# Performance work log

Hardware: AMD Instinct MI355X
Metric: run time of the kernel (lower is better)

Reference implementation:

```python
import jax, jax.numpy as jnp
import numpy as np

IN_DIM, EDGE_DIM, HID = 128, 64, 128
N_A, N_B, E_AB, E_AA = 50000, 50000, 320000, 320000


def setup_inputs() -> dict:
    key = jax.random.key(0)
    ks = jax.random.split(key, 13)
    inv = lambda n: 1.0 / np.sqrt(n)
    return {
        "x_a": jax.random.normal(ks[0], (N_A, IN_DIM), jnp.float32),
        "x_b": jax.random.normal(ks[1], (N_B, IN_DIM), jnp.float32),
        "ei_ab": jax.random.randint(ks[2], (2, E_AB), 0, N_A),
        "ea_ab": jax.random.normal(ks[3], (E_AB, EDGE_DIM), jnp.float32),
        "ei_aa": jax.random.randint(ks[4], (2, E_AA), 0, N_A),
        "ea_aa": jax.random.normal(ks[5], (E_AA, EDGE_DIM), jnp.float32),
        "Wh_w": jax.random.normal(ks[6], (EDGE_DIM, HID), jnp.float32) * inv(EDGE_DIM),
        "Wh_b": jnp.zeros((HID,), jnp.float32),
        "Wn_w": jax.random.normal(ks[7], (2 * IN_DIM, HID), jnp.float32) * inv(2 * IN_DIM),
        "Wn_b": jnp.zeros((HID,), jnp.float32),
        "w_e": jax.random.normal(ks[8], (HID,), jnp.float32) * inv(HID),
        "ft_w": jax.random.normal(ks[9], (IN_DIM, IN_DIM), jnp.float32) * inv(IN_DIM),
        "ft_b": jnp.zeros((IN_DIM,), jnp.float32),
    }


def reference(x_a, x_b, ei_ab, ea_ab, ei_aa, ea_aa,
              Wh_w, Wh_b, Wn_w, Wn_b, w_e, ft_w, ft_b):
    def edge_alpha(x_src, x_dst, ei, ea):
        # gather src/dst feats -> linear + relu -> score -> softmax over all edges
        s, d = ei[0], ei[1]
        nf = jnp.concatenate([x_src[s], x_dst[d]], axis=1)          # [E, 2*in_dim]
        h = jax.nn.relu(ea @ Wh_w + Wh_b + nf @ Wn_w + Wn_b)         # [E, hid]
        return jax.nn.softmax(h @ w_e, axis=0)                       # [E]

    alpha_ab = edge_alpha(x_a, x_b, ei_ab, ea_ab)
    alpha_aa = edge_alpha(x_a, x_a, ei_aa, ea_aa)

    lf_a = jnp.zeros_like(x_a)
    lf_b = jnp.zeros_like(x_b)
    s_ab, d_ab = ei_ab[0], ei_ab[1]
    # cross-type edge: scatter into both endpoint node types
    lf_a = lf_a.at[s_ab].add(-alpha_ab[:, None] * x_b[d_ab])
    lf_b = lf_b.at[d_ab].add(-alpha_ab[:, None] * x_a[s_ab])
    s_aa, d_aa = ei_aa[0], ei_aa[1]
    # same-type edge: single scatter (src side only, per original)
    lf_a = lf_a.at[s_aa].add(-alpha_aa[:, None] * x_a[d_aa])

    out_a = x_a + lf_a
    out_a = out_a + (out_a @ ft_w + ft_b)
    out_b = x_b + lf_b
    out_b = out_b + (out_b @ ft_w + ft_b)
    return out_a, out_b, alpha_ab, alpha_aa
```

## Files before the change

kernel.cpp:

```cpp
#include <hip/hip_runtime.h>
#include <hip/hip_fp16.h>
#include <cstdint>
#include <cstddef>

#define N_A   50000
#define N_B   50000
#define E_AB  320000
#define E_AA  320000
#define IN_DIM 128
#define HID    128
#define ED     64

using bf16x8 = __attribute__((ext_vector_type(8))) short;
using f32x4  = __attribute__((ext_vector_type(4))) float;
typedef unsigned short ushort_t;
typedef unsigned int   uint_t;

__device__ inline ushort_t bf16r(float f) {
    uint_t u = __float_as_uint(f);
    u = (u + 0x7FFF + ((u >> 16) & 1)) >> 16;
    return (ushort_t)u;
}
__device__ inline float bf2f(ushort_t h) {
    return __uint_as_float(((uint_t)h) << 16);
}
__device__ inline ushort_t f16r(float f) { return __half_as_ushort(__float2half_rn(f)); }
__device__ inline float f16f(ushort_t u) { return __half2float(__ushort_as_half(u)); }
__device__ inline uint_t packh2(float a, float b) {
    return (uint_t)f16r(a) | ((uint_t)f16r(b) << 16);
}

__device__ inline void online_merge(float& m, float& l, float om, float ol) {
    const float nm = fmaxf(m, om);
    l = l * __expf(m - nm) + ol * __expf(om - nm);
    m = nm;
}

__global__ __launch_bounds__(64) void prep_w_all(
    const float* __restrict__ Wh, const float* __restrict__ W1,
    const float* __restrict__ W2, const float* __restrict__ FT,
    const float* __restrict__ we,
    ushort_t* __restrict__ BhWh, ushort_t* __restrict__ BlWh,
    ushort_t* __restrict__ BhW1, ushort_t* __restrict__ BlW1,
    ushort_t* __restrict__ BhW2, ushort_t* __restrict__ BlW2,
    ushort_t* __restrict__ BhFT, ushort_t* __restrict__ BlFT,
    float* __restrict__ wep)
{
    const int f = blockIdx.x;
    const int lane = threadIdx.x;
    if (f == 112) {
#pragma unroll
        for (int q = 0; q < 2; ++q) {
            const int idx = lane + q * 64;
            const int l15 = idx >> 3, ct = idx & 7;
            wep[idx] = we[ct * 16 + l15];
        }
        return;
    }
    const float* W; ushort_t *oh, *ol; int KT, fl;
    if (f < 16)      { W = Wh; oh = BhWh; ol = BlWh; KT = 2; fl = f; }
    else if (f < 48) { W = W1; oh = BhW1; ol = BlW1; KT = 4; fl = f - 16; }
    else if (f < 80) { W = W2; oh = BhW2; ol = BlW2; KT = 4; fl = f - 48; }
    else             { W = FT; oh = BhFT; ol = BlFT; KT = 4; fl = f - 80; }
    const int ct = fl / KT, kt = fl % KT;
    const int col = ct * 16 + (lane & 15);
    const int kb  = kt * 32 + (lane >> 4) * 8;
#pragma unroll
    for (int j = 0; j < 8; ++j) {
        const float v = W[(kb + j) * 128 + col];
        const ushort_t h = bf16r(v);
        oh[(size_t)(fl * 64 + lane) * 8 + j] = h;
        ol[(size_t)(fl * 64 + lane) * 8 + j] = bf16r(v - bf2f(h));
    }
}

__global__ __launch_bounds__(256) void proj_dual_mfma(
    const float* __restrict__ X,
    const ushort_t* __restrict__ B1h, const ushort_t* __restrict__ B1l,
    const ushort_t* __restrict__ B2h, const ushort_t* __restrict__ B2l,
    const float* __restrict__ bh, const float* __restrict__ bn,
    ushort_t* __restrict__ P1, ushort_t* __restrict__ P2,
    ushort_t* __restrict__ X16, int N)
{
    const int lane = threadIdx.x & 63;
    const int l15 = lane & 15, lg = lane >> 4;
    const int r0 = blockIdx.x * 64 + (threadIdx.x >> 6) * 16;
    const int arow = (r0 + l15 < N) ? (r0 + l15) : (N - 1);

    bf16x8 ahi[4], alo[4];
#pragma unroll
    for (int kt = 0; kt < 4; ++kt) {
        float v[8];
        *(float4*)(v + 0) = *(const float4*)&X[(size_t)arow * 128 + kt * 32 + lg * 8];
        *(float4*)(v + 4) = *(const float4*)&X[(size_t)arow * 128 + kt * 32 + lg * 8 + 4];
        uint4 xu;
        xu.x = packh2(v[0], v[1]); xu.y = packh2(v[2], v[3]);
        xu.z = packh2(v[4], v[5]); xu.w = packh2(v[6], v[7]);
        *(uint4*)&X16[(size_t)arow * 128 + kt * 32 + lg * 8] = xu;
#pragma unroll
        for (int j = 0; j < 8; ++j) {
            const ushort_t h = bf16r(v[j]);
            ahi[kt][j] = (short)h;
            alo[kt][j] = (short)bf16r(v[j] - bf2f(h));
        }
    }

    f32x4 acc1[8], acc2[8];
#pragma unroll
    for (int ct = 0; ct < 8; ++ct) {
        const float b = bh[ct * 16 + l15] + bn[ct * 16 + l15];
        acc1[ct] = (f32x4){b, b, b, b};
        acc2[ct] = (f32x4){0.f, 0.f, 0.f, 0.f};
    }

#pragma unroll
    for (int ct = 0; ct < 8; ++ct) {
#pragma unroll
        for (int kt = 0; kt < 4; ++kt) {
            const size_t fo = (size_t)((ct * 4 + kt) * 64 + lane) * 8;
            const bf16x8 b1h = *(const bf16x8*)&B1h[fo];
            const bf16x8 b1l = *(const bf16x8*)&B1l[fo];
            const bf16x8 b2h = *(const bf16x8*)&B2h[fo];
            const bf16x8 b2l = *(const bf16x8*)&B2l[fo];
            acc1[ct] = __builtin_amdgcn_mfma_f32_16x16x32_bf16(ahi[kt], b1h, acc1[ct], 0, 0, 0);
            acc1[ct] = __builtin_amdgcn_mfma_f32_16x16x32_bf16(alo[kt], b1h, acc1[ct], 0, 0, 0);
            acc1[ct] = __builtin_amdgcn_mfma_f32_16x16x32_bf16(ahi[kt], b1l, acc1[ct], 0, 0, 0);
            acc2[ct] = __builtin_amdgcn_mfma_f32_16x16x32_bf16(ahi[kt], b2h, acc2[ct], 0, 0, 0);
            acc2[ct] = __builtin_amdgcn_mfma_f32_16x16x32_bf16(alo[kt], b2h, acc2[ct], 0, 0, 0);
            acc2[ct] = __builtin_amdgcn_mfma_f32_16x16x32_bf16(ahi[kt], b2l, acc2[ct], 0, 0, 0);
        }
    }
#pragma unroll
    for (int i = 0; i < 4; ++i) {
        const int row = r0 + lg * 4 + i;
        if (row < N) {
            uint4 u1, u2;
            u1.x = packh2(acc1[0][i], acc1[1][i]); u1.y = packh2(acc1[2][i], acc1[3][i]);
            u1.z = packh2(acc1[4][i], acc1[5][i]); u1.w = packh2(acc1[6][i], acc1[7][i]);
            u2.x = packh2(acc2[0][i], acc2[1][i]); u2.y = packh2(acc2[2][i], acc2[3][i]);
            u2.z = packh2(acc2[4][i], acc2[5][i]); u2.w = packh2(acc2[6][i], acc2[7][i]);
            *(uint4*)&P1[(size_t)row * 128 + l15 * 8] = u1;
            *(uint4*)&P2[(size_t)row * 128 + l15 * 8] = u2;
        }
    }
}

__global__ __launch_bounds__(256) void proj_single_mfma(
    const float* __restrict__ X,
    const ushort_t* __restrict__ Bh, const ushort_t* __restrict__ Bl,
    ushort_t* __restrict__ P, ushort_t* __restrict__ X16, int N)
{
    const int lane = threadIdx.x & 63;
    const int l15 = lane & 15, lg = lane >> 4;
    const int r0 = blockIdx.x * 64 + (threadIdx.x >> 6) * 16;
    const int arow = (r0 + l15 < N) ? (r0 + l15) : (N - 1);

    bf16x8 ahi[4], alo[4];
#pragma unroll
    for (int kt = 0; kt < 4; ++kt) {
        float v[8];
        *(float4*)(v + 0) = *(const float4*)&X[(size_t)arow * 128 + kt * 32 + lg * 8];
        *(float4*)(v + 4) = *(const float4*)&X[(size_t)arow * 128 + kt * 32 + lg * 8 + 4];
        uint4 xu;
        xu.x = packh2(v[0], v[1]); xu.y = packh2(v[2], v[3]);
        xu.z = packh2(v[4], v[5]); xu.w = packh2(v[6], v[7]);
        *(uint4*)&X16[(size_t)arow * 128 + kt * 32 + lg * 8] = xu;
#pragma unroll
        for (int j = 0; j < 8; ++j) {
            const ushort_t h = bf16r(v[j]);
            ahi[kt][j] = (short)h;
            alo[kt][j] = (short)bf16r(v[j] - bf2f(h));
        }
    }

    f32x4 acc[8];
#pragma unroll
    for (int ct = 0; ct < 8; ++ct) acc[ct] = (f32x4){0.f, 0.f, 0.f, 0.f};

#pragma unroll
    for (int ct = 0; ct < 8; ++ct) {
#pragma unroll
        for (int kt = 0; kt < 4; ++kt) {
            const size_t fo = (size_t)((ct * 4 + kt) * 64 + lane) * 8;
            const bf16x8 bhf = *(const bf16x8*)&Bh[fo];
            const bf16x8 blf = *(const bf16x8*)&Bl[fo];
            acc[ct] = __builtin_amdgcn_mfma_f32_16x16x32_bf16(ahi[kt], bhf, acc[ct], 0, 0, 0);
            acc[ct] = __builtin_amdgcn_mfma_f32_16x16x32_bf16(alo[kt], bhf, acc[ct], 0, 0, 0);
            acc[ct] = __builtin_amdgcn_mfma_f32_16x16x32_bf16(ahi[kt], blf, acc[ct], 0, 0, 0);
        }
    }
#pragma unroll
    for (int i = 0; i < 4; ++i) {
        const int row = r0 + lg * 4 + i;
        if (row < N) {
            uint4 u;
            u.x = packh2(acc[0][i], acc[1][i]); u.y = packh2(acc[2][i], acc[3][i]);
            u.z = packh2(acc[4][i], acc[5][i]); u.w = packh2(acc[6][i], acc[7][i]);
            *(uint4*)&P[(size_t)row * 128 + l15 * 8] = u;
        }
    }
}

__global__ __launch_bounds__(256) void edge_score_k(
    const float* __restrict__ ea_ab, const float* __restrict__ ea_aa,
    const int*   __restrict__ ei_ab, const int*   __restrict__ ei_aa,
    const ushort_t* __restrict__ P1h,
    const ushort_t* __restrict__ P2ah, const ushort_t* __restrict__ P2bh,
    const ushort_t* __restrict__ Bhi,  const ushort_t* __restrict__ Blo,
    const float* __restrict__ wep,
    float* __restrict__ scAB, float* __restrict__ scAA,
    int* __restrict__ cntA, int* __restrict__ cntB,
    int* __restrict__ rkAab, int* __restrict__ rkBab, int* __restrict__ rkAaa,
    float* __restrict__ pm, float* __restrict__ pl)
{
    const int t    = threadIdx.x;
    const int lane = t & 63;
    const int l15  = lane & 15;
    const int lg   = lane >> 4;
    const int wv   = t >> 6;
    const int type = (blockIdx.x >= 5000);
    const int bb   = type ? (blockIdx.x - 5000) : blockIdx.x;
    const int eb   = bb * 64;

    const float* __restrict__ ea  = type ? ea_aa : ea_ab;
    const int*   __restrict__ ei  = type ? ei_aa : ei_ab;
    const ushort_t* __restrict__ P2h = type ? P2ah : P2bh;
    float* __restrict__ score = type ? scAA : scAB;

    __shared__ ushort_t sBh[8192];
    __shared__ ushort_t sBl[8192];
    {
        const uint4* gh = (const uint4*)Bhi;
        const uint4* gl = (const uint4*)Blo;
        uint4* sh = (uint4*)sBh;
        uint4* sl = (uint4*)sBl;
#pragma unroll
        for (int i = 0; i < 4; ++i) {
            sh[t + i * 256] = gh[t + i * 256];
            sl[t + i * 256] = gl[t + i * 256];
        }
    }

    if (t < 64) {
        const int e = eb + t;
        const int s = ei[e];
        const int r = atomicAdd(&cntA[s], 1);
        if (type) rkAaa[e] = r; else rkAab[e] = r;
    } else if (t < 128 && !type) {
        const int e = eb + (t - 64);
        const int d = ei[(size_t)E_AB + e];
        rkBab[e] = atomicAdd(&cntB[d], 1);
    }

    const int e0 = eb + wv * 16;

    int sidx[4], didx[4];
#pragma unroll
    for (int i = 0; i < 4; ++i) {
        const int e = e0 + lg * 4 + i;
        sidx[i] = ei[e];
        didx[i] = ei[(size_t)E_AB + e];
    }
    uint4 p1u[4], p2u[4];
#pragma unroll
    for (int i = 0; i < 4; ++i) {
        p1u[i] = *(const uint4*)&P1h[(size_t)sidx[i] * 128 + l15 * 8];
        p2u[i] = *(const uint4*)&P2h[(size_t)didx[i] * 128 + l15 * 8];
    }

    const float* arow = &ea[(size_t)(e0 + l15) * 64 + lg * 8];
    float af[16];
    *(float4*)(af + 0)  = *(const float4*)(arow + 0);
    *(float4*)(af + 4)  = *(const float4*)(arow + 4);
    *(float4*)(af + 8)  = *(const float4*)(arow + 32);
    *(float4*)(af + 12) = *(const float4*)(arow + 36);

    bf16x8 ahi0, alo0, ahi1, alo1;
#pragma unroll
    for (int j = 0; j < 8; ++j) {
        const ushort_t h0 = bf16r(af[j]);
        ahi0[j] = (short)h0;
        alo0[j] = (short)bf16r(af[j] - bf2f(h0));
        const ushort_t h1 = bf16r(af[8 + j]);
        ahi1[j] = (short)h1;
        alo1[j] = (short)bf16r(af[8 + j] - bf2f(h1));
    }

    __syncthreads();

    f32x4 acc[8];
#pragma unroll
    for (int ct = 0; ct < 8; ++ct) acc[ct] = (f32x4){0.f, 0.f, 0.f, 0.f};

#pragma unroll
    for (int ct = 0; ct < 8; ++ct) {
        const bf16x8 bh0 = *(const bf16x8*)&sBh[(ct * 2 + 0) * 512 + lane * 8];
        const bf16x8 bl0 = *(const bf16x8*)&sBl[(ct * 2 + 0) * 512 + lane * 8];
        const bf16x8 bh1 = *(const bf16x8*)&sBh[(ct * 2 + 1) * 512 + lane * 8];
        const bf16x8 bl1 = *(const bf16x8*)&sBl[(ct * 2 + 1) * 512 + lane * 8];
        acc[ct] = __builtin_amdgcn_mfma_f32_16x16x32_bf16(ahi0, bh0, acc[ct], 0, 0, 0);
        acc[ct] = __builtin_amdgcn_mfma_f32_16x16x32_bf16(alo0, bh0, acc[ct], 0, 0, 0);
        acc[ct] = __builtin_amdgcn_mfma_f32_16x16x32_bf16(ahi0, bl0, acc[ct], 0, 0, 0);
        acc[ct] = __builtin_amdgcn_mfma_f32_16x16x32_bf16(ahi1, bh1, acc[ct], 0, 0, 0);
        acc[ct] = __builtin_amdgcn_mfma_f32_16x16x32_bf16(alo1, bh1, acc[ct], 0, 0, 0);
        acc[ct] = __builtin_amdgcn_mfma_f32_16x16x32_bf16(ahi1, bl1, acc[ct], 0, 0, 0);
    }

    float w8[8];
    *(float4*)(w8 + 0) = *(const float4*)&wep[l15 * 8];
    *(float4*)(w8 + 4) = *(const float4*)&wep[l15 * 8 + 4];

    float part[4];
#pragma unroll
    for (int i = 0; i < 4; ++i) {
        const __half2* h1 = (const __half2*)&p1u[i];
        const __half2* h2 = (const __half2*)&p2u[i];
        float p = 0.f;
#pragma unroll
        for (int q = 0; q < 4; ++q) {
            const float2 pf = __half22float2(__hadd2(h1[q], h2[q]));
            const float v0 = acc[2 * q][i] + pf.x;
            const float v1 = acc[2 * q + 1][i] + pf.y;
            p = fmaf(fmaxf(v0, 0.f), w8[2 * q], p);
            p = fmaf(fmaxf(v1, 0.f), w8[2 * q + 1], p);
        }
        part[i] = p;
    }
#pragma unroll
    for (int m = 8; m >= 1; m >>= 1) {
#pragma unroll
        for (int i = 0; i < 4; ++i) part[i] += __shfl_xor(part[i], m, 64);
    }
    if (l15 == 0) {
#pragma unroll
        for (int i = 0; i < 4; ++i) score[e0 + lg * 4 + i] = part[i];
    }

    float mw = fmaxf(fmaxf(part[0], part[1]), fmaxf(part[2], part[3]));
    float lw = __expf(part[0] - mw) + __expf(part[1] - mw)
             + __expf(part[2] - mw) + __expf(part[3] - mw);
#pragma unroll
    for (int off = 16; off <= 32; off <<= 1) {
        const float om = __shfl_xor(mw, off, 64);
        const float ol = __shfl_xor(lw, off, 64);
        online_merge(mw, lw, om, ol);
    }
    __shared__ float smm[4], sll[4];
    if (lane == 0) { smm[wv] = mw; sll[wv] = lw; }
    __syncthreads();
    if (t == 0) {
        float M = smm[0], L = sll[0];
        for (int i = 1; i < 4; ++i) online_merge(M, L, smm[i], sll[i]);
        pm[blockIdx.x] = M;
        pl[blockIdx.x] = L;
    }
}

__global__ __launch_bounds__(1024) void softmax_final_kernel(
    const float* __restrict__ pm, const float* __restrict__ pl,
    float* __restrict__ ML, int nPart)
{
    const int type = blockIdx.x;
    const float* mi = pm + type * nPart;
    const float* li = pl + type * nPart;
    float m = -1e30f, l = 0.f;
    for (int i = threadIdx.x; i < nPart; i += 1024) online_merge(m, l, mi[i], li[i]);
#pragma unroll
    for (int off = 1; off < 64; off <<= 1) {
        const float om = __shfl_xor(m, off, 64);
        const float ol = __shfl_xor(l, off, 64);
        online_merge(m, l, om, ol);
    }
    __shared__ float smm[16], sll[16];
    const int w = threadIdx.x >> 6, lane = threadIdx.x & 63;
    if (lane == 0) { smm[w] = m; sll[w] = l; }
    __syncthreads();
    if (threadIdx.x == 0) {
        float M = smm[0], L = sll[0];
        for (int i = 1; i < 16; ++i) online_merge(M, L, smm[i], sll[i]);
        ML[type * 2]     = M;
        ML[type * 2 + 1] = L;
    }
}

__global__ __launch_bounds__(1024) void csr_scan_kernel(
    const int* __restrict__ cntA, int* __restrict__ offA,
    const int* __restrict__ cntB, int* __restrict__ offB, int N)
{
    const int* cnt = (blockIdx.x == 0) ? cntA : cntB;
    int* off = (blockIdx.x == 0) ? offA : offB;

    __shared__ int warpsum[16];
    const int t = threadIdx.x, lane = t & 63, w = t >> 6;
    int carry = 0;

    for (int base = 0; base < N; base += 1024) {
        const int i = base + t;
        const int v = (i < N) ? cnt[i] : 0;
        int x = v;
#pragma unroll
        for (int d = 1; d < 64; d <<= 1) {
            const int y = __shfl_up(x, d, 64);
            if (lane >= d) x += y;
        }
        if (lane == 63) warpsum[w] = x;
        __syncthreads();
        if (w == 0 && lane < 16) {
            int s = warpsum[lane];
#pragma unroll
            for (int d = 1; d < 16; d <<= 1) {
                const int y = __shfl_up(s, d, 64);
                if (lane >= d) s += y;
            }
            warpsum[lane] = s;
        }
        __syncthreads();
        const int excl = (x - v) + ((w > 0) ? warpsum[w - 1] : 0) + carry;
        if (i < N) off[i] = excl;
        carry += warpsum[15];
        __syncthreads();
    }
    if (t == 0) off[N] = carry;
}

__global__ __launch_bounds__(256) void csr_fill_kernel(
    const int* __restrict__ ei_ab, const int* __restrict__ ei_aa,
    float* __restrict__ scAB, float* __restrict__ scAA,
    const float* __restrict__ ML,
    const int* __restrict__ offA, const int* __restrict__ offB,
    const int* __restrict__ rkAab, const int* __restrict__ rkBab,
    const int* __restrict__ rkAaa,
    int2* __restrict__ idxA, int2* __restrict__ idxB)
{
    const int i = blockIdx.x * 256 + threadIdx.x;
    const float Mab = ML[0], rLab = 1.0f / ML[1];
    const float Maa = ML[2], rLaa = 1.0f / ML[3];
    if (i < E_AB) {
        const float a = __expf(scAB[i] - Mab) * rLab;
        scAB[i] = a;
        const int s = ei_ab[i], d = ei_ab[E_AB + i];
        const int ab = __float_as_int(a);
        int pA = offA[s] + rkAab[i]; if (pA > 2 * E_AB - 1) pA = 2 * E_AB - 1;
        int pB = offB[d] + rkBab[i]; if (pB > E_AB - 1) pB = E_AB - 1;
        idxA[pA] = make_int2(d | (1 << 20), ab);
        idxB[pB] = make_int2(s, ab);
    }
    if (i < E_AA) {
        const float a = __expf(scAA[i] - Maa) * rLaa;
        scAA[i] = a;
        const int s = ei_aa[i];
        const int daa = ei_aa[E_AA + i];
        int pA = offA[s] + rkAaa[i]; if (pA > 2 * E_AB - 1) pA = 2 * E_AB - 1;
        idxA[pA] = make_int2(daa, __float_as_int(a));
    }
}

__global__ __launch_bounds__(256) void gather_final(
    const int*  __restrict__ off, const int2* __restrict__ idx,
    const ushort_t* __restrict__ xa16, const ushort_t* __restrict__ xb16,
    const float* __restrict__ xself,
    const ushort_t* __restrict__ Bh, const ushort_t* __restrict__ Bl,
    const float* __restrict__ fb,
    float* __restrict__ T, int N)
{
    const int lane = threadIdx.x & 63;
    const int l15  = lane & 15, lg = lane >> 4;
    const int wv   = threadIdx.x >> 6;
    const int r0   = blockIdx.x * 64 + wv * 16;

    for (int s = 0; s < 4; ++s) {
        const int row = r0 + s * 4 + lg;
        if (row < N) {
            const int beg = off[row], end = off[row + 1];
            float a8[8];
            *(float4*)(a8 + 0) = *(const float4*)&xself[(size_t)row * 128 + l15 * 8];
            *(float4*)(a8 + 4) = *(const float4*)&xself[(size_t)row * 128 + l15 * 8 + 4];
            int e = beg;
            for (; e + 3 < end; e += 4) {
                int2 q[4];
#pragma unroll
                for (int k = 0; k < 4; ++k) q[k] = idx[e + k];
                uint4 f[4];
#pragma unroll
                for (int k = 0; k < 4; ++k) {
                    const ushort_t* sp = (q[k].x & (1 << 20)) ? xb16 : xa16;
                    f[k] = *(const uint4*)&sp[(size_t)(q[k].x & 0xFFFFF) * 128 + l15 * 8];
                }
#pragma unroll
                for (int k = 0; k < 4; ++k) {
                    const float al = __int_as_float(q[k].y);
                    const __half2* hp = (const __half2*)&f[k];
#pragma unroll
                    for (int j = 0; j < 4; ++j) {
                        const float2 vf = __half22float2(hp[j]);
                        a8[2 * j]     = fmaf(-al, vf.x, a8[2 * j]);
                        a8[2 * j + 1] = fmaf(-al, vf.y, a8[2 * j + 1]);
                    }
                }
            }
            for (; e < end; ++e) {
                const int2 q0 = idx[e];
                const float al = __int_as_float(q0.y);
                const ushort_t* sp = (q0.x & (1 << 20)) ? xb16 : xa16;
                const uint4 f0 = *(const uint4*)&sp[(size_t)(q0.x & 0xFFFFF) * 128 + l15 * 8];
                const __half2* hp = (const __half2*)&f0;
#pragma unroll
                for (int j = 0; j < 4; ++j) {
                    const float2 vf = __half22float2(hp[j]);
                    a8[2 * j]     = fmaf(-al, vf.x, a8[2 * j]);
                    a8[2 * j + 1] = fmaf(-al, vf.y, a8[2 * j + 1]);
                }
            }
            *(float4*)&T[(size_t)row * 128 + l15 * 8]     = *(float4*)(a8 + 0);
            *(float4*)&T[(size_t)row * 128 + l15 * 8 + 4] = *(float4*)(a8 + 4);
        }
    }
    __syncthreads();

    const int arow = (r0 + l15 < N) ? (r0 + l15) : (N - 1);
    bf16x8 ahi[4], alo[4];
#pragma unroll
    for (int kt = 0; kt < 4; ++kt) {
        float v[8];
        *(float4*)(v + 0) = *(const float4*)&T[(size_t)arow * 128 + kt * 32 + lg * 8];
        *(float4*)(v + 4) = *(const float4*)&T[(size_t)arow * 128 + kt * 32 + lg * 8 + 4];
#pragma unroll
        for (int j = 0; j < 8; ++j) {
            const ushort_t h = bf16r(v[j]);
            ahi[kt][j] = (short)h;
            alo[kt][j] = (short)bf16r(v[j] - bf2f(h));
        }
    }

    f32x4 acc[8];
#pragma unroll
    for (int ct = 0; ct < 8; ++ct) {
        const float b = fb[ct * 16 + l15];
#pragma unroll
        for (int i = 0; i < 4; ++i) {
            const int row = r0 + lg * 4 + i;
            const int rr = (row < N) ? row : (N - 1);
            acc[ct][i] = T[(size_t)rr * 128 + ct * 16 + l15] + b;
        }
    }

#pragma unroll
    for (int ct = 0; ct < 8; ++ct) {
#pragma unroll
        for (int kt = 0; kt < 4; ++kt) {
            const size_t fo = (size_t)((ct * 4 + kt) * 64 + lane) * 8;
            const bf16x8 bhf = *(const bf16x8*)&Bh[fo];
            const bf16x8 blf = *(const bf16x8*)&Bl[fo];
            acc[ct] = __builtin_amdgcn_mfma_f32_16x16x32_bf16(ahi[kt], bhf, acc[ct], 0, 0, 0);
            acc[ct] = __builtin_amdgcn_mfma_f32_16x16x32_bf16(alo[kt], bhf, acc[ct], 0, 0, 0);
            acc[ct] = __builtin_amdgcn_mfma_f32_16x16x32_bf16(ahi[kt], blf, acc[ct], 0, 0, 0);
        }
    }
#pragma unroll
    for (int ct = 0; ct < 8; ++ct) {
#pragma unroll
        for (int i = 0; i < 4; ++i) {
            const int row = r0 + lg * 4 + i;
            if (row < N) T[(size_t)row * 128 + ct * 16 + l15] = acc[ct][i];
        }
    }
}

extern "C" void kernel_launch(void* const* d_in, const int* in_sizes, int n_in,
                              void* d_out, int out_size, void* d_ws, size_t ws_size,
                              hipStream_t stream)
{
    const float* x_a   = (const float*)d_in[0];
    const float* x_b   = (const float*)d_in[1];
    const int*   ei_ab = (const int*)d_in[2];
    const float* ea_ab = (const float*)d_in[3];
    const int*   ei_aa = (const int*)d_in[4];
    const float* ea_aa = (const float*)d_in[5];
    const float* Wh_w  = (const float*)d_in[6];
    const float* Wh_b  = (const float*)d_in[7];
    const float* Wn_w  = (const float*)d_in[8];
    const float* Wn_b  = (const float*)d_in[9];
    const float* w_e   = (const float*)d_in[10];
    const float* ft_w  = (const float*)d_in[11];
    const float* ft_b  = (const float*)d_in[12];

    float* out = (float*)d_out;
    float* ws  = (float*)d_ws;

    ushort_t* P1h  = (ushort_t*)(ws);
    ushort_t* P2ah = (ushort_t*)(ws + 3200000);
    ushort_t* P2bh = (ushort_t*)(ws + 6400000);
    ushort_t* xa16 = (ushort_t*)(ws + 9600000);
    ushort_t* xb16 = (ushort_t*)(ws + 12800000);
    int* rkAab = (int*)(ws + 16000000);
    int* rkBab = (int*)(ws + 16320000);
    int* rkAaa = (int*)(ws + 16640000);
    int* cntA  = (int*)(ws + 16960000);
    int* cntB  = (int*)(ws + 17010000);
    int* offA  = (int*)(ws + 17060000);
    int* offB  = (int*)(ws + 17110004);
    float* pm  = ws + 17160008;
    float* pl  = ws + 17170008;
    float* ML  = ws + 17180008;
    float* wep = ws + 17180016;
    ushort_t* FR = (ushort_t*)(ws + 17180208);
    ushort_t* BhWh = FR;
    ushort_t* BlWh = FR + 8192;
    ushort_t* BhW1 = FR + 16384;
    ushort_t* BlW1 = FR + 32768;
    ushort_t* BhW2 = FR + 49152;
    ushort_t* BlW2 = FR + 65536;
    ushort_t* BhFT = FR + 81920;
    ushort_t* BlFT = FR + 98304;
    int2* idxA = (int2*)(ws + 17240000);
    int2* idxB = (int2*)(ws + 18520000);

    float* TA   = out;
    float* TB   = out + 6400000;
    float* alAB = out + 12800000;
    float* alAA = out + 13120000;

    hipMemsetAsync(cntA, 0, 100000 * sizeof(int), stream);
    prep_w_all<<<113, 64, 0, stream>>>(Wh_w, Wn_w, Wn_w + 128 * 128, ft_w, w_e,
                                       BhWh, BlWh, BhW1, BlW1, BhW2, BlW2, BhFT, BlFT, wep);

    proj_dual_mfma<<<(N_A + 63) / 64, 256, 0, stream>>>(x_a, BhW1, BlW1, BhW2, BlW2,
                                                        Wh_b, Wn_b, P1h, P2ah, xa16, N_A);
    proj_single_mfma<<<(N_B + 63) / 64, 256, 0, stream>>>(x_b, BhW2, BlW2, P2bh, xb16, N_B);

    edge_score_k<<<10000, 256, 0, stream>>>(ea_ab, ea_aa, ei_ab, ei_aa,
                                            P1h, P2ah, P2bh, BhWh, BlWh, wep,
                                            alAB, alAA, cntA, cntB,
                                            rkAab, rkBab, rkAaa, pm, pl);

    softmax_final_kernel<<<2, 1024, 0, stream>>>(pm, pl, ML, 5000);

    csr_scan_kernel<<<2, 1024, 0, stream>>>(cntA, offA, cntB, offB, N_A);
    csr_fill_kernel<<<(E_AB + 255) / 256, 256, 0, stream>>>(ei_ab, ei_aa, alAB, alAA, ML,
                                                            offA, offB, rkAab, rkBab, rkAaa,
                                                            idxA, idxB);

    gather_final<<<(N_A + 63) / 64, 256, 0, stream>>>(offA, idxA, xa16, xb16, x_a,
                                                      BhFT, BlFT, ft_b, TA, N_A);
    gather_final<<<(N_B + 63) / 64, 256, 0, stream>>>(offB, idxB, xa16, xb16, x_b,
                                                      BhFT, BlFT, ft_b, TB, N_B);

    (void)in_sizes; (void)n_in; (void)out_size; (void)ws_size;
}
```

Measured before the change: 331.9 us.

## Loop edge tiles per wave with double-buffered gathers in edge scoring

Each wave now processes eight 16-edge tiles in a loop, prefetching the next tile's indices, edge attributes and projected node rows while computing the current one. Grid size drops eightfold, so the shared-memory weight staging is amortized over more edges and the per-block barrier for softmax partials is removed, with each wave writing its own online max/sum. The trade-off is fewer resident waves for hiding latency and higher register pressure from the double buffers.

New measurement: 366.5 us. 1.1x slower.

```diff
diff --git a/kernel.cpp b/kernel.cpp
--- a/kernel.cpp
+++ b/kernel.cpp
@@ -217,15 +217,16 @@
     const int lane = t & 63;
     const int l15  = lane & 15;
     const int lg   = lane >> 4;
-    const int wv   = t >> 6;
-    const int type = (blockIdx.x >= 5000);
-    const int bb   = type ? (blockIdx.x - 5000) : blockIdx.x;
-    const int eb   = bb * 64;
+    const int gw   = blockIdx.x * 4 + (t >> 6);
+    const int type = (gw >= 2500) ? 1 : 0;
+    const int wvi  = type ? (gw - 2500) : gw;
+    const long ebase = (long)wvi * 128;
 
     const float* __restrict__ ea  = type ? ea_aa : ea_ab;
     const int*   __restrict__ ei  = type ? ei_aa : ei_ab;
     const ushort_t* __restrict__ P2h = type ? P2ah : P2bh;
     float* __restrict__ score = type ? scAA : scAB;
+    int* __restrict__ rkA = type ? rkAaa : rkAab;
 
     __shared__ ushort_t sBh[8192];
     __shared__ ushort_t sBl[8192];
@@ -241,119 +242,137 @@
         }
     }
 
-    if (t < 64) {
-        const int e = eb + t;
-        const int s = ei[e];
-        const int r = atomicAdd(&cntA[s], 1);
-        if (type) rkAaa[e] = r; else rkAab[e] = r;
-    } else if (t < 128 && !type) {
-        const int e = eb + (t - 64);
-        const int d = ei[(size_t)E_AB + e];
-        rkBab[e] = atomicAdd(&cntB[d], 1);
-    }
-
-    const int e0 = eb + wv * 16;
-
-    int sidx[4], didx[4];
-#pragma unroll
-    for (int i = 0; i < 4; ++i) {
-        const int e = e0 + lg * 4 + i;
-        sidx[i] = ei[e];
-        didx[i] = ei[(size_t)E_AB + e];
-    }
-    uint4 p1u[4], p2u[4];
-#pragma unroll
-    for (int i = 0; i < 4; ++i) {
-        p1u[i] = *(const uint4*)&P1h[(size_t)sidx[i] * 128 + l15 * 8];
-        p2u[i] = *(const uint4*)&P2h[(size_t)didx[i] * 128 + l15 * 8];
-    }
-
-    const float* arow = &ea[(size_t)(e0 + l15) * 64 + lg * 8];
-    float af[16];
-    *(float4*)(af + 0)  = *(const float4*)(arow + 0);
-    *(float4*)(af + 4)  = *(const float4*)(arow + 4);
-    *(float4*)(af + 8)  = *(const float4*)(arow + 32);
-    *(float4*)(af + 12) = *(const float4*)(arow + 36);
-
-    bf16x8 ahi0, alo0, ahi1, alo1;
-#pragma unroll
-    for (int j = 0; j < 8; ++j) {
-        const ushort_t h0 = bf16r(af[j]);
-        ahi0[j] = (short)h0;
-        alo0[j] = (short)bf16r(af[j] - bf2f(h0));
-        const ushort_t h1 = bf16r(af[8 + j]);
-        ahi1[j] = (short)h1;
-        alo1[j] = (short)bf16r(af[8 + j] - bf2f(h1));
-    }
-
-    __syncthreads();
-
-    f32x4 acc[8];
-#pragma unroll
-    for (int ct = 0; ct < 8; ++ct) acc[ct] = (f32x4){0.f, 0.f, 0.f, 0.f};
-
-#pragma unroll
-    for (int ct = 0; ct < 8; ++ct) {
-        const bf16x8 bh0 = *(const bf16x8*)&sBh[(ct * 2 + 0) * 512 + lane * 8];
-        const bf16x8 bl0 = *(const bf16x8*)&sBl[(ct * 2 + 0) * 512 + lane * 8];
-        const bf16x8 bh1 = *(const bf16x8*)&sBh[(ct * 2 + 1) * 512 + lane * 8];
-        const bf16x8 bl1 = *(const bf16x8*)&sBl[(ct * 2 + 1) * 512 + lane * 8];
-        acc[ct] = __builtin_amdgcn_mfma_f32_16x16x32_bf16(ahi0, bh0, acc[ct], 0, 0, 0);
-        acc[ct] = __builtin_amdgcn_mfma_f32_16x16x32_bf16(alo0, bh0, acc[ct], 0, 0, 0);
-        acc[ct] = __builtin_amdgcn_mfma_f32_16x16x32_bf16(ahi0, bl0, acc[ct], 0, 0, 0);
-        acc[ct] = __builtin_amdgcn_mfma_f32_16x16x32_bf16(ahi1, bh1, acc[ct], 0, 0, 0);
-        acc[ct] = __builtin_amdgcn_mfma_f32_16x16x32_bf16(alo1, bh1, acc[ct], 0, 0, 0);
-        acc[ct] = __builtin_amdgcn_mfma_f32_16x16x32_bf16(ahi1, bl1, acc[ct], 0, 0, 0);
-    }
-
     float w8[8];
     *(float4*)(w8 + 0) = *(const float4*)&wep[l15 * 8];
     *(float4*)(w8 + 4) = *(const float4*)&wep[l15 * 8 + 4];
 
-    float part[4];
-#pragma unroll
-    for (int i = 0; i < 4; ++i) {
-        const __half2* h1 = (const __half2*)&p1u[i];
-        const __half2* h2 = (const __half2*)&p2u[i];
-        float p = 0.f;
-#pragma unroll
-        for (int q = 0; q < 4; ++q) {
-            const float2 pf = __half22float2(__hadd2(h1[q], h2[q]));
-            const float v0 = acc[2 * q][i] + pf.x;
-            const float v1 = acc[2 * q + 1][i] + pf.y;
-            p = fmaf(fmaxf(v0, 0.f), w8[2 * q], p);
-            p = fmaf(fmaxf(v1, 0.f), w8[2 * q + 1], p);
-        }
-        part[i] = p;
-    }
-#pragma unroll
-    for (int m = 8; m >= 1; m >>= 1) {
-#pragma unroll
-        for (int i = 0; i < 4; ++i) part[i] += __shfl_xor(part[i], m, 64);
-    }
-    if (l15 == 0) {
-#pragma unroll
-        for (int i = 0; i < 4; ++i) score[e0 + lg * 4 + i] = part[i];
-    }
-
-    float mw = fmaxf(fmaxf(part[0], part[1]), fmaxf(part[2], part[3]));
-    float lw = __expf(part[0] - mw) + __expf(part[1] - mw)
-             + __expf(part[2] - mw) + __expf(part[3] - mw);
-#pragma unroll
-    for (int off = 16; off <= 32; off <<= 1) {
-        const float om = __shfl_xor(mw, off, 64);
-        const float ol = __shfl_xor(lw, off, 64);
-        online_merge(mw, lw, om, ol);
-    }
-    __shared__ float smm[4], sll[4];
-    if (lane == 0) { smm[wv] = mw; sll[wv] = lw; }
+    int   sidx[2][4], didx[2][4];
+    uint4 p1u[2][4], p2u[2][4];
+    float af[2][16];
+
+    {
+#pragma unroll
+        for (int i = 0; i < 4; ++i) {
+            sidx[0][i] = ei[ebase + lg * 4 + i];
+            didx[0][i] = ei[(size_t)E_AB + ebase + lg * 4 + i];
+        }
+        const float* ar = &ea[(size_t)(ebase + l15) * 64 + lg * 8];
+        *(float4*)(af[0] + 0)  = *(const float4*)(ar + 0);
+        *(float4*)(af[0] + 4)  = *(const float4*)(ar + 4);
+        *(float4*)(af[0] + 8)  = *(const float4*)(ar + 32);
+        *(float4*)(af[0] + 12) = *(const float4*)(ar + 36);
+#pragma unroll
+        for (int i = 0; i < 4; ++i) {
+            p1u[0][i] = *(const uint4*)&P1h[(size_t)sidx[0][i] * 128 + l15 * 8];
+            p2u[0][i] = *(const uint4*)&P2h[(size_t)didx[0][i] * 128 + l15 * 8];
+        }
+    }
     __syncthreads();
-    if (t == 0) {
-        float M = smm[0], L = sll[0];
-        for (int i = 1; i < 4; ++i) online_merge(M, L, smm[i], sll[i]);
-        pm[blockIdx.x] = M;
-        pl[blockIdx.x] = L;
-    }
+
+    float mrun = -1e30f, lrun = 0.f;
+
+#pragma unroll 2
+    for (int k = 0; k < 8; ++k) {
+        const int cur = k & 1, nxt = cur ^ 1;
+        const long e0 = ebase + (long)k * 16;
+
+        if (k + 1 < 8) {
+            const long e1 = e0 + 16;
+#pragma unroll
+            for (int i = 0; i < 4; ++i) {
+                sidx[nxt][i] = ei[e1 + lg * 4 + i];
+                didx[nxt][i] = ei[(size_t)E_AB + e1 + lg * 4 + i];
+            }
+            const float* ar = &ea[(size_t)(e1 + l15) * 64 + lg * 8];
+            *(float4*)(af[nxt] + 0)  = *(const float4*)(ar + 0);
+            *(float4*)(af[nxt] + 4)  = *(const float4*)(ar + 4);
+            *(float4*)(af[nxt] + 8)  = *(const float4*)(ar + 32);
+            *(float4*)(af[nxt] + 12) = *(const float4*)(ar + 36);
+        }
+
+        bf16x8 ahi0, alo0, ahi1, alo1;
+#pragma unroll
+        for (int j = 0; j < 8; ++j) {
+            const float v0 = af[cur][j];
+            const ushort_t h0 = bf16r(v0);
+            ahi0[j] = (short)h0;
+            alo0[j] = (short)bf16r(v0 - bf2f(h0));
+            const float v1 = af[cur][8 + j];
+            const ushort_t h1 = bf16r(v1);
+            ahi1[j] = (short)h1;
+            alo1[j] = (short)bf16r(v1 - bf2f(h1));
+        }
+
+        f32x4 acc[8];
+#pragma unroll
+        for (int ct = 0; ct < 8; ++ct) acc[ct] = (f32x4){0.f, 0.f, 0.f, 0.f};
+#pragma unroll
+        for (int ct = 0; ct < 8; ++ct) {
+            const bf16x8 bh0 = *(const bf16x8*)&sBh[(ct * 2 + 0) * 512 + lane * 8];
+            const bf16x8 bl0 = *(const bf16x8*)&sBl[(ct * 2 + 0) * 512 + lane * 8];
+            const bf16x8 bh1 = *(const bf16x8*)&sBh[(ct * 2 + 1) * 512 + lane * 8];
+            const bf16x8 bl1 = *(const bf16x8*)&sBl[(ct * 2 + 1) * 512 + lane * 8];
+            acc[ct] = __builtin_amdgcn_mfma_f32_16x16x32_bf16(ahi0, bh0, acc[ct], 0, 0, 0);
+            acc[ct] = __builtin_amdgcn_mfma_f32_16x16x32_bf16(alo0, bh0, acc[ct], 0, 0, 0);
+            acc[ct] = __builtin_amdgcn_mfma_f32_16x16x32_bf16(ahi0, bl0, acc[ct], 0, 0, 0);
+            acc[ct] = __builtin_amdgcn_mfma_f32_16x16x32_bf16(ahi1, bh1, acc[ct], 0, 0, 0);
+            acc[ct] = __builtin_amdgcn_mfma_f32_16x16x32_bf16(alo1, bh1, acc[ct], 0, 0, 0);
+            acc[ct] = __builtin_amdgcn_mfma_f32_16x16x32_bf16(ahi1, bl1, acc[ct], 0, 0, 0);
+        }
+
+        if (k + 1 < 8) {
+#pragma unroll
+            for (int i = 0; i < 4; ++i) {
+                p1u[nxt][i] = *(const uint4*)&P1h[(size_t)sidx[nxt][i] * 128 + l15 * 8];
+                p2u[nxt][i] = *(const uint4*)&P2h[(size_t)didx[nxt][i] * 128 + l15 * 8];
+            }
+        }
+
+        float part[4];
+#pragma unroll
+        for (int i = 0; i < 4; ++i) {
+            const __half2* h1 = (const __half2*)&p1u[cur][i];
+            const __half2* h2 = (const __half2*)&p2u[cur][i];
+            float p = 0.f;
+#pragma unroll
+            for (int q = 0; q < 4; ++q) {
+                const float2 pf = __half22float2(__hadd2(h1[q], h2[q]));
+                p = fmaf(fmaxf(acc[2 * q][i] + pf.x, 0.f), w8[2 * q], p);
+                p = fmaf(fmaxf(acc[2 * q + 1][i] + pf.y, 0.f), w8[2 * q + 1], p);
+            }
+            part[i] = p;
+        }
+#pragma unroll
+        for (int m = 8; m >= 1; m >>= 1) {
+#pragma unroll
+            for (int i = 0; i < 4; ++i) part[i] += __shfl_xor(part[i], m, 64);
+        }
+        if (l15 == 0) {
+#pragma unroll
+            for (int i = 0; i < 4; ++i) score[e0 + lg * 4 + i] = part[i];
+        }
+
+        if (lane < 16) {
+            const int s = ei[e0 + lane];
+            rkA[e0 + lane] = atomicAdd(&cntA[s], 1);
+        } else if (lane < 32 && !type) {
+            const int d = ei[(size_t)E_AB + e0 + (lane - 16)];
+            rkBab[e0 + (lane - 16)] = atomicAdd(&cntB[d], 1);
+        }
+
+        float mw = fmaxf(fmaxf(part[0], part[1]), fmaxf(part[2], part[3]));
+        float lw = __expf(part[0] - mw) + __expf(part[1] - mw)
+                 + __expf(part[2] - mw) + __expf(part[3] - mw);
+#pragma unroll
+        for (int off = 16; off <= 32; off <<= 1) {
+            const float om = __shfl_xor(mw, off, 64);
+            const float ol = __shfl_xor(lw, off, 64);
+            online_merge(mw, lw, om, ol);
+        }
+        online_merge(mrun, lrun, mw, lw);
+    }
+
+    if (lane == 0) { pm[gw] = mrun; pl[gw] = lrun; }
 }
 
 __global__ __launch_bounds__(1024) void softmax_final_kernel(
@@ -600,10 +619,10 @@
     int* offA  = (int*)(ws + 17060000);
     int* offB  = (int*)(ws + 17110004);
     float* pm  = ws + 17160008;
-    float* pl  = ws + 17170008;
-    float* ML  = ws + 17180008;
-    float* wep = ws + 17180016;
-    ushort_t* FR = (ushort_t*)(ws + 17180208);
+    float* pl  = ws + 17165008;
+    float* ML  = ws + 17170008;
+    float* wep = ws + 17170016;
+    ushort_t* FR = (ushort_t*)(ws + 17170208);
     ushort_t* BhWh = FR;
     ushort_t* BlWh = FR + 8192;
     ushort_t* BhW1 = FR + 16384;
@@ -628,12 +647,12 @@
                                                         Wh_b, Wn_b, P1h, P2ah, xa16, N_A);
     proj_single_mfma<<<(N_B + 63) / 64, 256, 0, stream>>>(x_b, BhW2, BlW2, P2bh, xb16, N_B);
 
-    edge_score_k<<<10000, 256, 0, stream>>>(ea_ab, ea_aa, ei_ab, ei_aa,
-                                            P1h, P2ah, P2bh, BhWh, BlWh, wep,
-                                            alAB, alAA, cntA, cntB,
-                                            rkAab, rkBab, rkAaa, pm, pl);
-
-    softmax_final_kernel<<<2, 1024, 0, stream>>>(pm, pl, ML, 5000);
+    edge_score_k<<<1250, 256, 0, stream>>>(ea_ab, ea_aa, ei_ab, ei_aa,
+                                           P1h, P2ah, P2bh, BhWh, BlWh, wep,
+                                           alAB, alAA, cntA, cntB,
+                                           rkAab, rkBab, rkAaa, pm, pl);
+
+    softmax_final_kernel<<<2, 1024, 0, stream>>>(pm, pl, ML, 2500);
 
     csr_scan_kernel<<<2, 1024, 0, stream>>>(cntA, offA, cntB, offB, N_A);
     csr_fill_kernel<<<(E_AB + 255) / 256, 256, 0, stream>>>(ei_ab, ei_aa, alAB, alAA, ML,
```
